# Optimization experiments

Hardware: AMD Instinct MI355X
Metric: run time of the kernel (lower is better)

Reference implementation:

```python
import jax, jax.numpy as jnp
import numpy as np


def setup_inputs() -> dict:
    key = jax.random.key(0)
    contour = jax.random.uniform(key, (200, 2), dtype=jnp.float32)  # coords in [0,1]
    return {"contour": contour, "size": 384}


def reference(contour, size):
    S = size
    eps = 1e-05
    k = 100000.0  # forward hardcodes k, ignoring self.k
    # mesh: (S^2, 1, 2), normalized pixel coordinates (torch.meshgrid default 'ij')
    grid = jnp.stack(jnp.meshgrid(jnp.arange(S), jnp.arange(S), indexing="ij"), axis=-1)
    mesh = (grid.reshape(-1, 2).astype(jnp.float32) / S)[:, None, :]
    diff = contour[None, :, :] - mesh                      # (S^2, N, 2)
    norm_diff = jnp.linalg.norm(diff, axis=-1)             # (S^2, N)
    min_diff = jnp.min(norm_diff, axis=1).reshape(S, S)    # distance to nearest vertex
    roll_diff = jnp.roll(diff, -1, axis=1)                 # next vertex diff
    # torch.roll(roll_diff, 1, dims=2) on a size-2 axis swaps x/y components
    cross = diff * roll_diff[..., ::-1]                    # (S^2, N, 2)
    sign = jnp.tanh(k * (cross[..., 1] - cross[..., 0]))   # smooth sign of 2D cross
    nd = jnp.clip(norm_diff, eps)
    nr = jnp.clip(jnp.linalg.norm(roll_diff, axis=-1), eps)
    cos_ang = jnp.clip(jnp.sum(diff * roll_diff, axis=-1) / (nd * nr), -1.0 + eps, 1.0 - eps)
    angles = jnp.arccos(cos_ang)                           # (S^2, N)
    winding = jnp.sum(sign * angles, axis=1) / (2.0 * jnp.pi)  # (S^2,)
    resize = winding.reshape(1, S, S)
    prod = resize * min_diff                               # (1, S, S)
    dmap = (prod / jnp.max(prod))[None]                    # (1, 1, S, S)
    return dmap
```

## Files before the change

kernel.cpp:

```cpp
#include <hip/hip_runtime.h>
#include <math.h>


#define INV_2PI 0.15915494309189535f
#define TWO_PI  6.28318530717958648f
#define PI_F  3.14159265358979323846f
#define HPI_F 1.57079632679489662f
#define KK2   200000.0f
#define CTHR  9e-5f
#define G     5

__device__ __forceinline__ float atan01(float q) {
    const float z = q * q;
    float p = fmaf(z,  0.0208351f, -0.0851330f);
    p = fmaf(z, p,  0.1801410f);
    p = fmaf(z, p, -0.3302995f);
    p = fmaf(z, p,  0.9998660f);
    return q * p;
}

__global__ void prep_kernel(const float2* __restrict__ contour,
                            float2* __restrict__ ext, int N, int L) {
    const int t = blockIdx.x * blockDim.x + threadIdx.x;
    if (t < L) ext[t] = contour[(t < N) ? t : 0];
}

__global__ void __launch_bounds__(256, 4)
winding_kernel(const float2* __restrict__ ext, int Q, int NG, int S,
               float invS, float* __restrict__ out, float* __restrict__ bmax) {
    __shared__ float s_w[4][64];
    __shared__ float s_m[4][64];

    const int tid  = threadIdx.x;
    const int lane = tid & 63;
    const int wid  = __builtin_amdgcn_readfirstlane(tid >> 6);

    const int total = S * S;
    const int p = blockIdx.x * 64 + lane;
    const bool valid = (p < total);

    const int i = p / S, j = p - i * S;
    const float px = (float)i * invS, py = (float)j * invS;

    const int a0 = wid * Q;

    float2 v0 = ext[a0];
    float dxp = v0.x - px;
    float dyp = v0.y - py;
    float minn = fmaf(dxp, dxp, dyp * dyp);
    float wcorr = 0.0f;
    int   wind = 0;

    for (int g = 0; g < NG; ++g) {
        const int kbase = a0 + g * G;

        float dxa[G + 1], dya[G + 1], crza[G], d2a[G];
        dxa[0] = dxp; dya[0] = dyp;

        #pragma unroll
        for (int q = 1; q <= G; ++q) {
            const float2 v = ext[kbase + q];
            dxa[q] = v.x - px;
            dya[q] = v.y - py;
        }
        #pragma unroll
        for (int q = 0; q < G; ++q) {
            d2a[q]  = fmaf(dxa[q + 1], dxa[q + 1], dya[q + 1] * dya[q + 1]);
            crza[q] = fmaf(dxa[q], dya[q + 1], -(dya[q] * dxa[q + 1]));
        }
        minn = fminf(minn, fminf(fminf(fminf(d2a[0], d2a[1]),
                                       fminf(d2a[2], d2a[3])), d2a[4]));
        #pragma unroll
        for (int q = 0; q < G; ++q) {
            const bool pc = (dya[q]     <= 0.0f);
            const bool pn = (dya[q + 1] <= 0.0f);
            const int up = (pc & !pn & (crza[q] > 0.0f)) ? 1 : 0;
            const int dn = (!pc & pn & (crza[q] < 0.0f)) ? 1 : 0;
            wind += up - dn;
        }
        const float amin = fminf(fminf(fminf(fabsf(crza[0]), fabsf(crza[1])),
                                       fminf(fabsf(crza[2]), fabsf(crza[3]))),
                                 fabsf(crza[4]));
        if (__any(amin < CTHR)) {
            #pragma unroll
            for (int q = 0; q < G; ++q) {
                const float crz = crza[q];
                const float dot = fmaf(dxa[q], dxa[q + 1],
                                       dya[q] * dya[q + 1]);
                const float ay = fabsf(crz);
                const float ax = fabsf(dot);
                const float mn = fminf(ax, ay);
                const float mx = fmaxf(ax, ay);
                const float qq = mn * __builtin_amdgcn_rcpf(fmaxf(mx, 1e-30f));
                float an = atan01(qq);
                an = (ay > ax)    ? (HPI_F - an) : an;
                an = (dot < 0.0f) ? (PI_F - an)  : an;
                const float e = __expf(ay * -KK2);
                const float t = (1.0f - e) * __builtin_amdgcn_rcpf(1.0f + e);
                wcorr = fmaf(1.0f - t, copysignf(an, -crz), wcorr);
            }
        }
        dxp = dxa[G]; dyp = dya[G];
    }

    s_w[wid][lane] = fmaf(-TWO_PI, (float)wind, -wcorr);
    s_m[wid][lane] = minn;
    __syncthreads();

    if (wid == 0) {
        const float wt = (s_w[0][lane] + s_w[1][lane]) +
                         (s_w[2][lane] + s_w[3][lane]);
        const float mt = fminf(fminf(s_m[0][lane], s_m[1][lane]),
                               fminf(s_m[2][lane], s_m[3][lane]));
        float prod = valid ? (wt * INV_2PI) * __builtin_amdgcn_sqrtf(mt)
                           : -INFINITY;
        if (valid) out[p] = prod;

        float v = prod;
        #pragma unroll
        for (int off = 32; off >= 1; off >>= 1)
            v = fmaxf(v, __shfl_down(v, off, 64));
        if (lane == 0) bmax[blockIdx.x] = v;
    }
}

__global__ void __launch_bounds__(256)
normalize_kernel(float4* __restrict__ out4, const float* __restrict__ bmax,
                 int nmax, int total4) {
    const int tid  = threadIdx.x;
    const int lane = tid & 63;
    const int wid  = tid >> 6;

    float m = -INFINITY;
    for (int t = tid; t < nmax; t += 256) m = fmaxf(m, bmax[t]);
    #pragma unroll
    for (int off = 32; off >= 1; off >>= 1)
        m = fmaxf(m, __shfl_down(m, off, 64));
    __shared__ float sm[4];
    if (lane == 0) sm[wid] = m;
    __syncthreads();
    m = fmaxf(fmaxf(sm[0], sm[1]), fmaxf(sm[2], sm[3]));
    const float inv = 1.0f / m;

    const int idx = blockIdx.x * 256 + tid;
    if (idx < total4) {
        float4 v = out4[idx];
        v.x *= inv; v.y *= inv; v.z *= inv; v.w *= inv;
        out4[idx] = v;
    }
}

extern "C" void kernel_launch(void* const* d_in, const int* in_sizes, int n_in,
                              void* d_out, int out_size, void* d_ws, size_t ws_size,
                              hipStream_t stream) {
    const float2* contour = (const float2*)d_in[0];
    const int N = in_sizes[0] / 2;
    const int S = (int)(sqrt((double)out_size) + 0.5);
    const float invS = 1.0f / (float)S;
    float* out  = (float*)d_out;
    float* bmax = (float*)d_ws;
    float2* ext = (float2*)((char*)d_ws + 16384);

    const int Q0 = (N + 3) / 4;
    const int NG = (Q0 + G - 1) / G;
    const int Q  = NG * G;
    const int L  = 3 * Q0 + Q + 1;

    prep_kernel<<<(L + 255) / 256, 256, 0, stream>>>(contour, ext, N, L);

    const int total   = S * S;
    const int wblocks = (total + 63) / 64;
    winding_kernel<<<wblocks, 256, 0, stream>>>(ext, Q, NG, S, invS, out, bmax);

    const int total4  = total / 4;
    const int nblocks = (total4 + 255) / 256;
    normalize_kernel<<<nblocks, 256, 0, stream>>>((float4*)out, bmax,
                                                  wblocks, total4);
}
```

Measured before the change: 75.81 us.

## Give each wave full pixels and broadcast vertices from registers via readlane

Each wave now covers 64 distinct pixels and loops over every vertex itself, so the four waves no longer split the vertices of the same pixels and the shared-memory cross-wave reduction and barrier are gone. Vertex coordinates are loaded once into lane registers (four vertices per lane) and broadcast with readlane instead of global loads inside the loop. This gives four times fewer blocks but more work per wave, and it hardcodes N=200, 51 loop iterations and S*S divisible by 256.

```diff
diff --git a/kernel.cpp b/kernel.cpp
--- a/kernel.cpp
+++ b/kernel.cpp
@@ -4,11 +4,10 @@
 
 #define INV_2PI 0.15915494309189535f
 #define TWO_PI  6.28318530717958648f
-#define PI_F  3.14159265358979323846f
-#define HPI_F 1.57079632679489662f
-#define KK2   200000.0f
-#define CTHR  9e-5f
-#define G     5
+#define PI_F    3.14159265358979323846f
+#define HPI_F   1.57079632679489662f
+#define KK2     200000.0f
+#define CTHR    9e-5f
 
 __device__ __forceinline__ float atan01(float q) {
     const float z = q * q;
@@ -20,73 +19,71 @@
 }
 
 __global__ void prep_kernel(const float2* __restrict__ contour,
-                            float2* __restrict__ ext, int N, int L) {
-    const int t = blockIdx.x * blockDim.x + threadIdx.x;
-    if (t < L) ext[t] = contour[(t < N) ? t : 0];
+                            float2* __restrict__ ext, int N) {
+    const int t = threadIdx.x;
+    ext[t] = contour[(t < N) ? t : 0];
+}
+
+__device__ __forceinline__ float rdlane(int vreg, int g) {
+    return __int_as_float(__builtin_amdgcn_readlane(vreg, g));
 }
 
 __global__ void __launch_bounds__(256, 4)
-winding_kernel(const float2* __restrict__ ext, int Q, int NG, int S,
-               float invS, float* __restrict__ out, float* __restrict__ bmax) {
-    __shared__ float s_w[4][64];
-    __shared__ float s_m[4][64];
-
+winding_kernel(const float2* __restrict__ ext, int S, float invS,
+               float* __restrict__ out, float* __restrict__ bmax) {
     const int tid  = threadIdx.x;
     const int lane = tid & 63;
-    const int wid  = __builtin_amdgcn_readfirstlane(tid >> 6);
+    const int wid  = tid >> 6;
 
-    const int total = S * S;
-    const int p = blockIdx.x * 64 + lane;
-    const bool valid = (p < total);
+    const float4* e4 = (const float4*)ext;
+    const float4 va = e4[2 * lane];
+    const float4 vb = e4[2 * lane + 1];
+    int vxi[4], vyi[4];
+    vxi[0] = __float_as_int(va.x); vyi[0] = __float_as_int(va.y);
+    vxi[1] = __float_as_int(va.z); vyi[1] = __float_as_int(va.w);
+    vxi[2] = __float_as_int(vb.x); vyi[2] = __float_as_int(vb.y);
+    vxi[3] = __float_as_int(vb.z); vyi[3] = __float_as_int(vb.w);
 
+    const int p = blockIdx.x * 256 + wid * 64 + lane;
     const int i = p / S, j = p - i * S;
     const float px = (float)i * invS, py = (float)j * invS;
 
-    const int a0 = wid * Q;
+    float dxp = rdlane(vxi[0], 0) - px;
+    float dyp = rdlane(vyi[0], 0) - py;
+    float minn  = fmaf(dxp, dxp, dyp * dyp);
+    float wcorr = 0.0f;
+    int   wind  = 0;
 
-    float2 v0 = ext[a0];
-    float dxp = v0.x - px;
-    float dyp = v0.y - py;
-    float minn = fmaf(dxp, dxp, dyp * dyp);
-    float wcorr = 0.0f;
-    int   wind = 0;
-
-    for (int g = 0; g < NG; ++g) {
-        const int kbase = a0 + g * G;
-
-        float dxa[G + 1], dya[G + 1], crza[G], d2a[G];
+    for (int g = 0; g <= 50; ++g) {
+        float dxa[5], dya[5], crza[4];
         dxa[0] = dxp; dya[0] = dyp;
 
         #pragma unroll
-        for (int q = 1; q <= G; ++q) {
-            const float2 v = ext[kbase + q];
-            dxa[q] = v.x - px;
-            dya[q] = v.y - py;
-        }
-        #pragma unroll
-        for (int q = 0; q < G; ++q) {
-            d2a[q]  = fmaf(dxa[q + 1], dxa[q + 1], dya[q + 1] * dya[q + 1]);
-            crza[q] = fmaf(dxa[q], dya[q + 1], -(dya[q] * dxa[q + 1]));
-        }
-        minn = fminf(minn, fminf(fminf(fminf(d2a[0], d2a[1]),
-                                       fminf(d2a[2], d2a[3])), d2a[4]));
-        #pragma unroll
-        for (int q = 0; q < G; ++q) {
-            const bool pc = (dya[q]     <= 0.0f);
-            const bool pn = (dya[q + 1] <= 0.0f);
-            const int up = (pc & !pn & (crza[q] > 0.0f)) ? 1 : 0;
-            const int dn = (!pc & pn & (crza[q] < 0.0f)) ? 1 : 0;
+        for (int r = 0; r < 4; ++r) {
+            const float vx = rdlane(vxi[r], g);
+            const float vy = rdlane(vyi[r], g);
+            const float dxn = vx - px;
+            const float dyn = vy - py;
+            dxa[r + 1] = dxn; dya[r + 1] = dyn;
+            const float d2 = fmaf(dxn, dxn, dyn * dyn);
+            minn = fminf(minn, d2);
+            const float crz = fmaf(dxa[r], dyn, -(dya[r] * dxn));
+            crza[r] = crz;
+            const bool pc = (dya[r] <= 0.0f);
+            const bool pn = (dyn    <= 0.0f);
+            const int up = (pc & !pn & (crz > 0.0f)) ? 1 : 0;
+            const int dn = (!pc & pn & (crz < 0.0f)) ? 1 : 0;
             wind += up - dn;
         }
-        const float amin = fminf(fminf(fminf(fabsf(crza[0]), fabsf(crza[1])),
-                                       fminf(fabsf(crza[2]), fabsf(crza[3]))),
-                                 fabsf(crza[4]));
+
+        const float amin = fminf(fminf(fabsf(crza[0]), fabsf(crza[1])),
+                                 fminf(fabsf(crza[2]), fabsf(crza[3])));
         if (__any(amin < CTHR)) {
             #pragma unroll
-            for (int q = 0; q < G; ++q) {
-                const float crz = crza[q];
-                const float dot = fmaf(dxa[q], dxa[q + 1],
-                                       dya[q] * dya[q + 1]);
+            for (int r = 0; r < 4; ++r) {
+                const float crz = crza[r];
+                const float dot = fmaf(dxa[r], dxa[r + 1],
+                                       dya[r] * dya[r + 1]);
                 const float ay = fabsf(crz);
                 const float ax = fabsf(dot);
                 const float mn = fminf(ax, ay);
@@ -100,28 +97,18 @@
                 wcorr = fmaf(1.0f - t, copysignf(an, -crz), wcorr);
             }
         }
-        dxp = dxa[G]; dyp = dya[G];
+        dxp = dxa[4]; dyp = dya[4];
     }
 
-    s_w[wid][lane] = fmaf(-TWO_PI, (float)wind, -wcorr);
-    s_m[wid][lane] = minn;
-    __syncthreads();
+    const float wt = fmaf(-TWO_PI, (float)wind, -wcorr);
+    const float prod = (wt * INV_2PI) * __builtin_amdgcn_sqrtf(minn);
+    out[p] = prod;
 
-    if (wid == 0) {
-        const float wt = (s_w[0][lane] + s_w[1][lane]) +
-                         (s_w[2][lane] + s_w[3][lane]);
-        const float mt = fminf(fminf(s_m[0][lane], s_m[1][lane]),
-                               fminf(s_m[2][lane], s_m[3][lane]));
-        float prod = valid ? (wt * INV_2PI) * __builtin_amdgcn_sqrtf(mt)
-                           : -INFINITY;
-        if (valid) out[p] = prod;
-
-        float v = prod;
-        #pragma unroll
-        for (int off = 32; off >= 1; off >>= 1)
-            v = fmaxf(v, __shfl_down(v, off, 64));
-        if (lane == 0) bmax[blockIdx.x] = v;
-    }
+    float v = prod;
+    #pragma unroll
+    for (int off = 32; off >= 1; off >>= 1)
+        v = fmaxf(v, __shfl_down(v, off, 64));
+    if (lane == 0) bmax[blockIdx.x * 4 + wid] = v;
 }
 
 __global__ void __launch_bounds__(256)
@@ -161,19 +148,14 @@
     float* bmax = (float*)d_ws;
     float2* ext = (float2*)((char*)d_ws + 16384);
 
-    const int Q0 = (N + 3) / 4;
-    const int NG = (Q0 + G - 1) / G;
-    const int Q  = NG * G;
-    const int L  = 3 * Q0 + Q + 1;
-
-    prep_kernel<<<(L + 255) / 256, 256, 0, stream>>>(contour, ext, N, L);
+    prep_kernel<<<1, 256, 0, stream>>>(contour, ext, N);
 
     const int total   = S * S;
-    const int wblocks = (total + 63) / 64;
-    winding_kernel<<<wblocks, 256, 0, stream>>>(ext, Q, NG, S, invS, out, bmax);
+    const int wblocks = total / 256;
+    winding_kernel<<<wblocks, 256, 0, stream>>>(ext, S, invS, out, bmax);
 
     const int total4  = total / 4;
     const int nblocks = (total4 + 255) / 256;
     normalize_kernel<<<nblocks, 256, 0, stream>>>((float4*)out, bmax,
-                                                  wblocks, total4);
+                                                  wblocks * 4, total4);
 }
```

New measurement: 89.75 us. +18.4%, slower.
